# Performance work log

Hardware: AMD Instinct MI355X
Metric: run time of the kernel (lower is better)

Reference implementation:

```python
import jax, jax.numpy as jnp
import numpy as np

N, NB = 256, 8732  # batch, default boxes (SSD300)


def setup_inputs() -> dict:
    key = jax.random.key(0)
    k1, k2, k3, k4, k5 = jax.random.split(key, 5)
    ploc = jax.random.normal(k1, (N, 4, NB), dtype=jnp.float32)
    plabel = jax.random.normal(k2, (N, 1, NB), dtype=jnp.float32)
    # gloc / dboxes need strictly positive w,h (log / division); offset uniform
    gloc = jax.random.uniform(k3, (N, 4, NB), dtype=jnp.float32) + 0.1
    glabel = jax.random.randint(k4, (N, NB), 0, 2).astype(jnp.int64)
    dboxes = jax.random.uniform(k5, (1, 4, NB), dtype=jnp.float32) + 0.1
    return {"ploc": ploc, "plabel": plabel, "gloc": gloc,
            "glabel": glabel, "dboxes": dboxes}


def _bce_logits(x, y):
    # numerically stable BCEWithLogits, reduction='none'
    return jnp.maximum(x, 0.0) - x * y + jnp.log1p(jnp.exp(-jnp.abs(x)))


def _smooth_l1(d):
    ad = jnp.abs(d)
    return jnp.where(ad < 1.0, 0.5 * d * d, ad - 0.5)


def reference(ploc, plabel, gloc, glabel, dboxes):
    scale_xy = 1.0
    scale_wh = 1.0
    mask = glabel > 0                              # [N, NB] bool
    pos_num = mask.sum(axis=1)                     # [N] int

    # location target vector
    gxy = scale_xy * (gloc[:, :2, :] - dboxes[:, :2, :]) / dboxes[:, 2:, :]
    gwh = scale_wh * jnp.log(gloc[:, 2:, :] / dboxes[:, 2:, :])
    vec_gd = jnp.concatenate((gxy, gwh), axis=1)   # [N, 4, NB]

    sl1 = _smooth_l1(ploc - vec_gd).sum(axis=1)    # [N, NB]
    sl1 = (mask.astype(sl1.dtype) * sl1).sum(axis=1)  # [N]

    pl = plabel.squeeze(1).astype(jnp.float32)     # [N, NB]
    gl = glabel.astype(jnp.float32)
    con = _bce_logits(pl, gl)                      # [N, NB]

    # hard negative mining: rank negatives by loss, keep top 3*pos_num
    con_neg = jnp.where(mask, 0.0, con)
    con_idx = jnp.argsort(-con_neg, axis=1)        # descending sort indices
    con_rank = jnp.argsort(con_idx, axis=1)        # rank of each position
    neg_num = jnp.clip(3 * pos_num, None, NB)[:, None]
    neg_mask = con_rank < neg_num                  # [N, NB] bool

    keep = (mask | neg_mask).astype(con.dtype)
    closs = (con * keep).sum(axis=1)               # [N]

    total_loss = sl1 + closs
    num_mask = (pos_num > 0).astype(total_loss.dtype)
    pos_f = jnp.clip(pos_num.astype(total_loss.dtype), 1e-6, None)
    return (total_loss * num_mask / pos_f).mean(axis=0)
```

## Files before the change

kernel.cpp:

```cpp
#include <hip/hip_runtime.h>
#include <math.h>

#define N_ROWS 256
#define NB 8732
#define NB4 2183
#define CHUNKS 9

typedef float f4 __attribute__((ext_vector_type(4)));
typedef int   i4 __attribute__((ext_vector_type(4)));

__device__ __forceinline__ float smooth_l1(float d) {
    float ad = fabsf(d);
    return ad < 1.0f ? 0.5f * d * d : ad - 0.5f;
}

__device__ __forceinline__ float bce_y0(float x) {
    return fmaxf(x, 0.0f) + log1pf(expf(-fabsf(x)));
}

__global__ __launch_bounds__(256) void partial_kernel(
    const float* __restrict__ ploc, const float* __restrict__ plabel,
    const float* __restrict__ gloc, const int* __restrict__ glabel,
    const float* __restrict__ dboxes, float* __restrict__ ws) {
    const int row = blockIdx.x;
    const int chunk = blockIdx.y;
    const int tid = threadIdx.x;
    const int g = chunk * 256 + tid;

    float sl1acc = 0.0f, conAll = 0.0f, conPos = 0.0f, posCnt = 0.0f;

    if (g < NB4) {
        const f4* __restrict__ ploc4 = (const f4*)ploc;
        const f4* __restrict__ gloc4 = (const f4*)gloc;
        const f4* __restrict__ db4   = (const f4*)dboxes;
        const f4* __restrict__ pl4   = (const f4*)plabel;
        const i4* __restrict__ gl4   = (const i4*)glabel;

        const int rb = row * 4 * NB4;
        const int rs = row * NB4;

        f4 p0 = ploc4[rb + 0 * NB4 + g];
        f4 p1 = ploc4[rb + 1 * NB4 + g];
        f4 p2 = ploc4[rb + 2 * NB4 + g];
        f4 p3 = ploc4[rb + 3 * NB4 + g];
        f4 q0 = gloc4[rb + 0 * NB4 + g];
        f4 q1 = gloc4[rb + 1 * NB4 + g];
        f4 q2 = gloc4[rb + 2 * NB4 + g];
        f4 q3 = gloc4[rb + 3 * NB4 + g];
        f4 d0 = db4[0 * NB4 + g];
        f4 d1 = db4[1 * NB4 + g];
        f4 d2 = db4[2 * NB4 + g];
        f4 d3 = db4[3 * NB4 + g];
        i4 lb = gl4[rs + g];
        f4 px = pl4[rs + g];

#pragma unroll
        for (int k = 0; k < 4; ++k) {
            float rw2 = __builtin_amdgcn_rcpf(d2[k]);
            float rw3 = __builtin_amdgcn_rcpf(d3[k]);
            float gx = (q0[k] - d0[k]) * rw2;
            float gy = (q1[k] - d1[k]) * rw3;
            float gw = __logf(q2[k] * rw2);
            float gh = __logf(q3[k] * rw3);
            float s = smooth_l1(p0[k] - gx)
                    + smooth_l1(p1[k] - gy)
                    + smooth_l1(p2[k] - gw)
                    + smooth_l1(p3[k] - gh);
            int lab = lb[k];
            float x = px[k];
            float con = fmaxf(x, 0.0f) - x * (float)lab
                      + __logf(1.0f + __expf(-fabsf(x)));
            conAll += con;
            float m = (lab > 0) ? 1.0f : 0.0f;
            posCnt += m;
            sl1acc += m * s;
            conPos += m * con;
        }
    }

    float v0 = sl1acc, v1 = conAll, v2 = conPos, v3 = posCnt;
#pragma unroll
    for (int off = 32; off > 0; off >>= 1) {
        v0 += __shfl_down(v0, off);
        v1 += __shfl_down(v1, off);
        v2 += __shfl_down(v2, off);
        v3 += __shfl_down(v3, off);
    }
    __shared__ float sm[4][4];
    const int wid = tid >> 6, lane = tid & 63;
    if (lane == 0) {
        sm[wid][0] = v0; sm[wid][1] = v1; sm[wid][2] = v2; sm[wid][3] = v3;
    }
    __syncthreads();
    if (tid == 0) {
        f4 part;
        part.x = sm[0][0] + sm[1][0] + sm[2][0] + sm[3][0];
        part.y = sm[0][1] + sm[1][1] + sm[2][1] + sm[3][1];
        part.z = sm[0][2] + sm[1][2] + sm[2][2] + sm[3][2];
        part.w = sm[0][3] + sm[1][3] + sm[2][3] + sm[3][3];
        ((f4*)ws)[chunk * N_ROWS + row] = part;
    }
}

__global__ __launch_bounds__(256) void final_kernel(
    const float* __restrict__ ws, const float* __restrict__ plabel,
    const int* __restrict__ glabel, float* __restrict__ out) {
    const int r = threadIdx.x;
    float sl1 = 0.f, cAll = 0.f, cPos = 0.f, posf = 0.f;
#pragma unroll
    for (int c = 0; c < CHUNKS; ++c) {
        f4 p = ((const f4*)ws)[c * N_ROWS + r];
        sl1 += p.x; cAll += p.y; cPos += p.z; posf += p.w;
    }
    const int pos = (int)(posf + 0.5f);
    const long long K = 3LL * (long long)pos;

    float closs;
    if (pos == 0) {
        closs = 0.0f;
    } else if (K >= (long long)NB) {
        closs = cAll;
    } else {
        const int Ki = (int)K;
        const float* plRow = plabel + r * NB;
        const int* glRow = glabel + r * NB;
        unsigned cur = 0;
        for (int bit = 31; bit >= 0; --bit) {
            unsigned trial = cur | (1u << bit);
            int c2 = 0;
            for (int j = 0; j < NB; ++j) {
                if (glRow[j] > 0) continue;
                float con = bce_y0(plRow[j]);
                if (__float_as_uint(con) >= trial) c2++;
            }
            if (c2 >= Ki) cur = trial;
        }
        const float thr = __uint_as_float(cur);
        int cntG = 0; float sumG = 0.f;
        for (int j = 0; j < NB; ++j) {
            if (glRow[j] > 0) continue;
            float con = bce_y0(plRow[j]);
            if (con > thr) { cntG++; sumG += con; }
        }
        closs = cPos + sumG + (float)(Ki - cntG) * thr;
    }

    float loss = (pos > 0) ? (sl1 + closs) / (float)pos : 0.0f;

#pragma unroll
    for (int off = 32; off > 0; off >>= 1) loss += __shfl_down(loss, off);
    __shared__ float sm[4];
    const int wid = threadIdx.x >> 6, lane = threadIdx.x & 63;
    if (lane == 0) sm[wid] = loss;
    __syncthreads();
    if (threadIdx.x == 0) {
        out[0] = (sm[0] + sm[1] + sm[2] + sm[3]) * (1.0f / 256.0f);
    }
}

extern "C" void kernel_launch(void* const* d_in, const int* in_sizes, int n_in,
                              void* d_out, int out_size, void* d_ws, size_t ws_size,
                              hipStream_t stream) {
    const float* ploc   = (const float*)d_in[0];
    const float* plabel = (const float*)d_in[1];
    const float* gloc   = (const float*)d_in[2];
    const int*   glabel = (const int*)d_in[3];
    const float* dboxes = (const float*)d_in[4];
    float* ws  = (float*)d_ws;
    float* out = (float*)d_out;

    dim3 grid(N_ROWS, CHUNKS);
    hipLaunchKernelGGL(partial_kernel, grid, dim3(256), 0, stream,
                       ploc, plabel, gloc, glabel, dboxes, ws);
    hipLaunchKernelGGL(final_kernel, dim3(1), dim3(256), 0, stream,
                       ws, plabel, glabel, out);
}
```

Before: 22.52 us.

## Fuse partial and final kernels into one per-row kernel with atomic output

Replaces the two-kernel scheme (a 256x9 grid of partial-sum blocks plus a single-block finalizer) with one kernel that assigns a 1024-thread block to each row. Each thread handles up to three vec4 batches. After a block reduction, lane 0 runs the hard-negative threshold search for its row and atomically adds that row's loss to the output. This removes the second launch and the workspace round trip, and spreads the serial mining work across 256 blocks instead of running it in one block. It adds a memset launch and a float atomic, which makes the summation order nondeterministic.

```diff
diff --git a/kernel.cpp b/kernel.cpp
--- a/kernel.cpp
+++ b/kernel.cpp
@@ -4,7 +4,8 @@
 #define N_ROWS 256
 #define NB 8732
 #define NB4 2183
-#define CHUNKS 9
+#define BT 1024
+#define TAIL (NB4 - 2 * BT)
 
 typedef float f4 __attribute__((ext_vector_type(4)));
 typedef int   i4 __attribute__((ext_vector_type(4)));
@@ -18,67 +19,87 @@
     return fmaxf(x, 0.0f) + log1pf(expf(-fabsf(x)));
 }
 
-__global__ __launch_bounds__(256) void partial_kernel(
+struct Batch {
+    f4 p0, p1, p2, p3, q0, q1, q2, q3, d0, d1, d2, d3, px;
+    i4 lb;
+};
+
+__device__ __forceinline__ Batch loadB(
+    const f4* __restrict__ ploc4, const f4* __restrict__ gloc4,
+    const f4* __restrict__ db4, const f4* __restrict__ pl4,
+    const i4* __restrict__ gl4, int rb, int rs, int g) {
+    Batch b;
+    b.p0 = ploc4[rb + 0 * NB4 + g];
+    b.p1 = ploc4[rb + 1 * NB4 + g];
+    b.p2 = ploc4[rb + 2 * NB4 + g];
+    b.p3 = ploc4[rb + 3 * NB4 + g];
+    b.q0 = gloc4[rb + 0 * NB4 + g];
+    b.q1 = gloc4[rb + 1 * NB4 + g];
+    b.q2 = gloc4[rb + 2 * NB4 + g];
+    b.q3 = gloc4[rb + 3 * NB4 + g];
+    b.d0 = db4[0 * NB4 + g];
+    b.d1 = db4[1 * NB4 + g];
+    b.d2 = db4[2 * NB4 + g];
+    b.d3 = db4[3 * NB4 + g];
+    b.lb = gl4[rs + g];
+    b.px = pl4[rs + g];
+    return b;
+}
+
+__device__ __forceinline__ void accumB(const Batch& b, float& sl1, float& cAll,
+                                       float& cPos, float& pCnt) {
+#pragma unroll
+    for (int k = 0; k < 4; ++k) {
+        float rw2 = __builtin_amdgcn_rcpf(b.d2[k]);
+        float rw3 = __builtin_amdgcn_rcpf(b.d3[k]);
+        float gx = (b.q0[k] - b.d0[k]) * rw2;
+        float gy = (b.q1[k] - b.d1[k]) * rw3;
+        float gw = __logf(b.q2[k] * rw2);
+        float gh = __logf(b.q3[k] * rw3);
+        float s = smooth_l1(b.p0[k] - gx)
+                + smooth_l1(b.p1[k] - gy)
+                + smooth_l1(b.p2[k] - gw)
+                + smooth_l1(b.p3[k] - gh);
+        int lab = b.lb[k];
+        float x = b.px[k];
+        float con = fmaxf(x, 0.0f) - x * (float)lab
+                  + __logf(1.0f + __expf(-fabsf(x)));
+        cAll += con;
+        float m = (lab > 0) ? 1.0f : 0.0f;
+        pCnt += m;
+        sl1 += m * s;
+        cPos += m * con;
+    }
+}
+
+__global__ __launch_bounds__(BT, 4) void row_kernel(
     const float* __restrict__ ploc, const float* __restrict__ plabel,
     const float* __restrict__ gloc, const int* __restrict__ glabel,
-    const float* __restrict__ dboxes, float* __restrict__ ws) {
+    const float* __restrict__ dboxes, float* __restrict__ out) {
     const int row = blockIdx.x;
-    const int chunk = blockIdx.y;
     const int tid = threadIdx.x;
-    const int g = chunk * 256 + tid;
 
-    float sl1acc = 0.0f, conAll = 0.0f, conPos = 0.0f, posCnt = 0.0f;
+    const f4* __restrict__ ploc4 = (const f4*)ploc;
+    const f4* __restrict__ gloc4 = (const f4*)gloc;
+    const f4* __restrict__ db4   = (const f4*)dboxes;
+    const f4* __restrict__ pl4   = (const f4*)plabel;
+    const i4* __restrict__ gl4   = (const i4*)glabel;
 
-    if (g < NB4) {
-        const f4* __restrict__ ploc4 = (const f4*)ploc;
-        const f4* __restrict__ gloc4 = (const f4*)gloc;
-        const f4* __restrict__ db4   = (const f4*)dboxes;
-        const f4* __restrict__ pl4   = (const f4*)plabel;
-        const i4* __restrict__ gl4   = (const i4*)glabel;
+    const int rb = row * 4 * NB4;
+    const int rs = row * NB4;
 
-        const int rb = row * 4 * NB4;
-        const int rs = row * NB4;
+    float sl1 = 0.f, cAll = 0.f, cPos = 0.f, pCnt = 0.f;
 
-        f4 p0 = ploc4[rb + 0 * NB4 + g];
-        f4 p1 = ploc4[rb + 1 * NB4 + g];
-        f4 p2 = ploc4[rb + 2 * NB4 + g];
-        f4 p3 = ploc4[rb + 3 * NB4 + g];
-        f4 q0 = gloc4[rb + 0 * NB4 + g];
-        f4 q1 = gloc4[rb + 1 * NB4 + g];
-        f4 q2 = gloc4[rb + 2 * NB4 + g];
-        f4 q3 = gloc4[rb + 3 * NB4 + g];
-        f4 d0 = db4[0 * NB4 + g];
-        f4 d1 = db4[1 * NB4 + g];
-        f4 d2 = db4[2 * NB4 + g];
-        f4 d3 = db4[3 * NB4 + g];
-        i4 lb = gl4[rs + g];
-        f4 px = pl4[rs + g];
-
-#pragma unroll
-        for (int k = 0; k < 4; ++k) {
-            float rw2 = __builtin_amdgcn_rcpf(d2[k]);
-            float rw3 = __builtin_amdgcn_rcpf(d3[k]);
-            float gx = (q0[k] - d0[k]) * rw2;
-            float gy = (q1[k] - d1[k]) * rw3;
-            float gw = __logf(q2[k] * rw2);
-            float gh = __logf(q3[k] * rw3);
-            float s = smooth_l1(p0[k] - gx)
-                    + smooth_l1(p1[k] - gy)
-                    + smooth_l1(p2[k] - gw)
-                    + smooth_l1(p3[k] - gh);
-            int lab = lb[k];
-            float x = px[k];
-            float con = fmaxf(x, 0.0f) - x * (float)lab
-                      + __logf(1.0f + __expf(-fabsf(x)));
-            conAll += con;
-            float m = (lab > 0) ? 1.0f : 0.0f;
-            posCnt += m;
-            sl1acc += m * s;
-            conPos += m * con;
-        }
+    Batch b0 = loadB(ploc4, gloc4, db4, pl4, gl4, rb, rs, tid);
+    Batch b1 = loadB(ploc4, gloc4, db4, pl4, gl4, rb, rs, tid + BT);
+    accumB(b0, sl1, cAll, cPos, pCnt);
+    accumB(b1, sl1, cAll, cPos, pCnt);
+    if (tid < TAIL) {
+        Batch b2 = loadB(ploc4, gloc4, db4, pl4, gl4, rb, rs, tid + 2 * BT);
+        accumB(b2, sl1, cAll, cPos, pCnt);
     }
 
-    float v0 = sl1acc, v1 = conAll, v2 = conPos, v3 = posCnt;
+    float v0 = sl1, v1 = cAll, v2 = cPos, v3 = pCnt;
 #pragma unroll
     for (int off = 32; off > 0; off >>= 1) {
         v0 += __shfl_down(v0, off);
@@ -86,75 +107,58 @@
         v2 += __shfl_down(v2, off);
         v3 += __shfl_down(v3, off);
     }
-    __shared__ float sm[4][4];
+    __shared__ float sm[16][4];
     const int wid = tid >> 6, lane = tid & 63;
     if (lane == 0) {
         sm[wid][0] = v0; sm[wid][1] = v1; sm[wid][2] = v2; sm[wid][3] = v3;
     }
     __syncthreads();
-    if (tid == 0) {
-        f4 part;
-        part.x = sm[0][0] + sm[1][0] + sm[2][0] + sm[3][0];
-        part.y = sm[0][1] + sm[1][1] + sm[2][1] + sm[3][1];
-        part.z = sm[0][2] + sm[1][2] + sm[2][2] + sm[3][2];
-        part.w = sm[0][3] + sm[1][3] + sm[2][3] + sm[3][3];
-        ((f4*)ws)[chunk * N_ROWS + row] = part;
-    }
-}
-
-__global__ __launch_bounds__(256) void final_kernel(
-    const float* __restrict__ ws, const float* __restrict__ plabel,
-    const int* __restrict__ glabel, float* __restrict__ out) {
-    const int r = threadIdx.x;
-    float sl1 = 0.f, cAll = 0.f, cPos = 0.f, posf = 0.f;
+    if (wid == 0) {
+        float a0 = 0.f, a1 = 0.f, a2 = 0.f, a3 = 0.f;
+        if (lane < 16) { a0 = sm[lane][0]; a1 = sm[lane][1];
+                         a2 = sm[lane][2]; a3 = sm[lane][3]; }
 #pragma unroll
-    for (int c = 0; c < CHUNKS; ++c) {
-        f4 p = ((const f4*)ws)[c * N_ROWS + r];
-        sl1 += p.x; cAll += p.y; cPos += p.z; posf += p.w;
-    }
-    const int pos = (int)(posf + 0.5f);
-    const long long K = 3LL * (long long)pos;
-
-    float closs;
-    if (pos == 0) {
-        closs = 0.0f;
-    } else if (K >= (long long)NB) {
-        closs = cAll;
-    } else {
-        const int Ki = (int)K;
-        const float* plRow = plabel + r * NB;
-        const int* glRow = glabel + r * NB;
-        unsigned cur = 0;
-        for (int bit = 31; bit >= 0; --bit) {
-            unsigned trial = cur | (1u << bit);
-            int c2 = 0;
-            for (int j = 0; j < NB; ++j) {
-                if (glRow[j] > 0) continue;
-                float con = bce_y0(plRow[j]);
-                if (__float_as_uint(con) >= trial) c2++;
+        for (int off = 8; off > 0; off >>= 1) {
+            a0 += __shfl_down(a0, off);
+            a1 += __shfl_down(a1, off);
+            a2 += __shfl_down(a2, off);
+            a3 += __shfl_down(a3, off);
+        }
+        if (lane == 0) {
+            const int pos = (int)(a3 + 0.5f);
+            const long long K = 3LL * (long long)pos;
+            float closs;
+            if (pos == 0) {
+                closs = 0.0f;
+            } else if (K >= (long long)NB) {
+                closs = a1;
+            } else {
+                const int Ki = (int)K;
+                const float* plRow = plabel + row * NB;
+                const int* glRow = glabel + row * NB;
+                unsigned cur = 0;
+                for (int bit = 31; bit >= 0; --bit) {
+                    unsigned trial = cur | (1u << bit);
+                    int c2 = 0;
+                    for (int j = 0; j < NB; ++j) {
+                        if (glRow[j] > 0) continue;
+                        float con = bce_y0(plRow[j]);
+                        if (__float_as_uint(con) >= trial) c2++;
+                    }
+                    if (c2 >= Ki) cur = trial;
+                }
+                const float thr = __uint_as_float(cur);
+                int cntG = 0; float sumG = 0.f;
+                for (int j = 0; j < NB; ++j) {
+                    if (glRow[j] > 0) continue;
+                    float con = bce_y0(plRow[j]);
+                    if (con > thr) { cntG++; sumG += con; }
+                }
+                closs = a2 + sumG + (float)(Ki - cntG) * thr;
             }
-            if (c2 >= Ki) cur = trial;
+            float loss = (pos > 0) ? (a0 + closs) / (float)pos : 0.0f;
+            atomicAdd(out, loss * (1.0f / 256.0f));
         }
-        const float thr = __uint_as_float(cur);
-        int cntG = 0; float sumG = 0.f;
-        for (int j = 0; j < NB; ++j) {
-            if (glRow[j] > 0) continue;
-            float con = bce_y0(plRow[j]);
-            if (con > thr) { cntG++; sumG += con; }
-        }
-        closs = cPos + sumG + (float)(Ki - cntG) * thr;
-    }
-
-    float loss = (pos > 0) ? (sl1 + closs) / (float)pos : 0.0f;
-
-#pragma unroll
-    for (int off = 32; off > 0; off >>= 1) loss += __shfl_down(loss, off);
-    __shared__ float sm[4];
-    const int wid = threadIdx.x >> 6, lane = threadIdx.x & 63;
-    if (lane == 0) sm[wid] = loss;
-    __syncthreads();
-    if (threadIdx.x == 0) {
-        out[0] = (sm[0] + sm[1] + sm[2] + sm[3]) * (1.0f / 256.0f);
     }
 }
 
@@ -166,12 +170,10 @@
     const float* gloc   = (const float*)d_in[2];
     const int*   glabel = (const int*)d_in[3];
     const float* dboxes = (const float*)d_in[4];
-    float* ws  = (float*)d_ws;
     float* out = (float*)d_out;
 
-    dim3 grid(N_ROWS, CHUNKS);
-    hipLaunchKernelGGL(partial_kernel, grid, dim3(256), 0, stream,
-                       ploc, plabel, gloc, glabel, dboxes, ws);
-    hipLaunchKernelGGL(final_kernel, dim3(1), dim3(256), 0, stream,
-                       ws, plabel, glabel, out);
+    hipMemsetAsync(out, 0, sizeof(float), stream);
+
+    hipLaunchKernelGGL(row_kernel, dim3(N_ROWS), dim3(BT), 0, stream,
+                       ploc, plabel, gloc, glabel, dboxes, out);
 }
```

New measurement: 27.74 us. 23.2% more time.

## Fuse final reduction into partial kernel via last-block-per-row atomic counter

Applied to the files above, without the earlier changes.

Replaces the two-kernel pipeline with one kernel. Each block atomically accumulates its partial sums into a per-row slot and bumps an arrival counter, and the last block of each row runs the hard-negative threshold search and atomically adds the row's loss to the output. This removes the second launch and spreads the per-row selection work across 256 blocks instead of one block's threads. In exchange it adds two memsets, float atomics that make the sum order nondeterministic, and a serial per-row search on a single lane.

```diff
diff --git a/kernel.cpp b/kernel.cpp
--- a/kernel.cpp
+++ b/kernel.cpp
@@ -5,6 +5,8 @@
 #define NB 8732
 #define NB4 2183
 #define CHUNKS 9
+#define SLOT_F 32
+#define WS_BYTES (N_ROWS * 128)
 
 typedef float f4 __attribute__((ext_vector_type(4)));
 typedef int   i4 __attribute__((ext_vector_type(4)));
@@ -18,10 +20,11 @@
     return fmaxf(x, 0.0f) + log1pf(expf(-fabsf(x)));
 }
 
-__global__ __launch_bounds__(256) void partial_kernel(
+__global__ __launch_bounds__(256) void fused_kernel(
     const float* __restrict__ ploc, const float* __restrict__ plabel,
     const float* __restrict__ gloc, const int* __restrict__ glabel,
-    const float* __restrict__ dboxes, float* __restrict__ ws) {
+    const float* __restrict__ dboxes, float* __restrict__ ws,
+    float* __restrict__ out) {
     const int row = blockIdx.x;
     const int chunk = blockIdx.y;
     const int tid = threadIdx.x;
@@ -92,29 +95,31 @@
         sm[wid][0] = v0; sm[wid][1] = v1; sm[wid][2] = v2; sm[wid][3] = v3;
     }
     __syncthreads();
-    if (tid == 0) {
-        f4 part;
-        part.x = sm[0][0] + sm[1][0] + sm[2][0] + sm[3][0];
-        part.y = sm[0][1] + sm[1][1] + sm[2][1] + sm[3][1];
-        part.z = sm[0][2] + sm[1][2] + sm[2][2] + sm[3][2];
-        part.w = sm[0][3] + sm[1][3] + sm[2][3] + sm[3][3];
-        ((f4*)ws)[chunk * N_ROWS + row] = part;
+    if (wid != 0) return;
+
+    float* slot = ws + row * SLOT_F;
+    unsigned* cntp = (unsigned*)(slot + 4);
+    if (lane < 4) {
+        float v = sm[0][lane] + sm[1][lane] + sm[2][lane] + sm[3][lane];
+        float old = atomicAdd(&slot[lane], v);
+        asm volatile("" :: "v"(old));
     }
-}
+    asm volatile("s_waitcnt vmcnt(0)" ::: "memory");
+    unsigned arr = 0;
+    if (lane == 0) arr = atomicAdd(cntp, 1u);
+    arr = __shfl(arr, 0);
+    if (arr != CHUNKS - 1) return;
 
-__global__ __launch_bounds__(256) void final_kernel(
-    const float* __restrict__ ws, const float* __restrict__ plabel,
-    const int* __restrict__ glabel, float* __restrict__ out) {
-    const int r = threadIdx.x;
-    float sl1 = 0.f, cAll = 0.f, cPos = 0.f, posf = 0.f;
-#pragma unroll
-    for (int c = 0; c < CHUNKS; ++c) {
-        f4 p = ((const f4*)ws)[c * N_ROWS + r];
-        sl1 += p.x; cAll += p.y; cPos += p.z; posf += p.w;
-    }
+    float rv = 0.0f;
+    if (lane < 4) rv = atomicAdd(&slot[lane], 0.0f);
+    float sl1  = __shfl(rv, 0);
+    float cAll = __shfl(rv, 1);
+    float cPos = __shfl(rv, 2);
+    float posf = __shfl(rv, 3);
+    if (lane != 0) return;
+
     const int pos = (int)(posf + 0.5f);
     const long long K = 3LL * (long long)pos;
-
     float closs;
     if (pos == 0) {
         closs = 0.0f;
@@ -122,8 +127,8 @@
         closs = cAll;
     } else {
         const int Ki = (int)K;
-        const float* plRow = plabel + r * NB;
-        const int* glRow = glabel + r * NB;
+        const float* plRow = plabel + row * NB;
+        const int* glRow = glabel + row * NB;
         unsigned cur = 0;
         for (int bit = 31; bit >= 0; --bit) {
             unsigned trial = cur | (1u << bit);
@@ -144,18 +149,8 @@
         }
         closs = cPos + sumG + (float)(Ki - cntG) * thr;
     }
-
     float loss = (pos > 0) ? (sl1 + closs) / (float)pos : 0.0f;
-
-#pragma unroll
-    for (int off = 32; off > 0; off >>= 1) loss += __shfl_down(loss, off);
-    __shared__ float sm[4];
-    const int wid = threadIdx.x >> 6, lane = threadIdx.x & 63;
-    if (lane == 0) sm[wid] = loss;
-    __syncthreads();
-    if (threadIdx.x == 0) {
-        out[0] = (sm[0] + sm[1] + sm[2] + sm[3]) * (1.0f / 256.0f);
-    }
+    atomicAdd(out, loss * (1.0f / 256.0f));
 }
 
 extern "C" void kernel_launch(void* const* d_in, const int* in_sizes, int n_in,
@@ -169,9 +164,10 @@
     float* ws  = (float*)d_ws;
     float* out = (float*)d_out;
 
+    hipMemsetAsync(ws, 0, WS_BYTES, stream);
+    hipMemsetAsync(out, 0, sizeof(float), stream);
+
     dim3 grid(N_ROWS, CHUNKS);
-    hipLaunchKernelGGL(partial_kernel, grid, dim3(256), 0, stream,
-                       ploc, plabel, gloc, glabel, dboxes, ws);
-    hipLaunchKernelGGL(final_kernel, dim3(1), dim3(256), 0, stream,
-                       ws, plabel, glabel, out);
+    hipLaunchKernelGGL(fused_kernel, grid, dim3(256), 0, stream,
+                       ploc, plabel, gloc, glabel, dboxes, ws, out);
 }
```

After: 28.85 us. 28.1% more time.
